# Optimization experiments

Hardware: AMD Instinct MI355X
Metric: run time of the kernel (lower is better)

Reference implementation:

```python
import jax, jax.numpy as jnp
import numpy as np


def setup_inputs() -> dict:
    key = jax.random.key(0)
    k0, k1, k2 = jax.random.split(key, 3)
    B, N, C = 2, 2048, 1024
    x = jax.random.normal(k0, (B, N, C), jnp.float32)
    W_qkv = jax.random.normal(k1, (3 * C, C), jnp.float32) * 0.02
    b_qkv = jnp.zeros((3 * C,), jnp.float32)
    W_out = jax.random.normal(k2, (C, C), jnp.float32) * 0.02
    b_out = jnp.zeros((C,), jnp.float32)
    return {"x": x, "W_qkv": W_qkv, "b_qkv": b_qkv, "W_out": W_out, "b_out": b_out, "n_heads": 16}


def reference(x, W_qkv, b_qkv, W_out, b_out, n_heads):
    B, N, C = x.shape
    dk = C // n_heads
    scale = 1.0 / np.sqrt(dk)
    # qkv projection -> (3, B, H, N, dk)
    qkv = (x @ W_qkv.T + b_qkv).reshape(B, N, 3, n_heads, dk).transpose(2, 0, 3, 1, 4)
    q, k, v = qkv[0], qkv[1], qkv[2]
    attn_all = jnp.einsum('bhqd,bhkd->bhqk', q, k) * scale  # (B,H,N,N)
    # sparsity measure per query row: max - mean
    M = jnp.max(attn_all, axis=-1) - jnp.mean(attn_all, axis=-1)  # (B,H,N)
    n_top = max(1, min(int(N * 0.25), N - 1))
    _, top_idx = jax.lax.top_k(M, n_top)  # (B,H,n_top)
    # keep[b,h,q] = True iff query row q is among top rows (vectorized scatter,
    # replaces the original per-(b,h) python loop)
    b_idx = jnp.arange(B)[:, None, None]
    h_idx = jnp.arange(n_heads)[None, :, None]
    keep = jnp.zeros((B, n_heads, N), bool).at[b_idx, h_idx, top_idx].set(True)
    # non-top query rows are fully masked to -1e9 (as in masked_fill)
    attn = jnp.where(keep[..., None], attn_all, jnp.float32(-1e9))
    attn = jax.nn.softmax(attn, axis=-1)
    # dropout is identity in eval mode
    out = jnp.einsum('bhqk,bhkd->bhqd', attn, v)
    out = out.transpose(0, 2, 1, 3).reshape(B, N, C)
    return out @ W_out.T + b_out
```

## Files before the change

kernel.cpp:

```cpp
#include <hip/hip_runtime.h>
#include <math.h>

typedef unsigned short u16;
typedef __attribute__((ext_vector_type(8))) short short8v;
typedef __attribute__((ext_vector_type(4))) float f32x4;

constexpr int B  = 2;
constexpr int N  = 2048;
constexpr int C  = 1024;
constexpr int H  = 16;
constexpr int DK = 64;
constexpr int NTOP = 512;
constexpr float SCALE = 0.125f;
constexpr int   BAND_CAP = 1024;
constexpr float BAND_EPS = 2e-3f;
constexpr int   CSEG = 16;

__device__ __forceinline__ void gload16(const u16* g, u16* l) {
    __builtin_amdgcn_global_load_lds(
        (const __attribute__((address_space(1))) unsigned int*)g,
        (__attribute__((address_space(3))) unsigned int*)l,
        16, 0, 0);
}

__device__ __forceinline__ u16 bf16_rne(float x) {
    unsigned u = __float_as_uint(x);
    unsigned r = u + 0x7fffu + ((u >> 16) & 1u);
    return (u16)(r >> 16);
}

__global__ __launch_bounds__(256) void convert_hilo(
    const float* __restrict__ src, u16* __restrict__ hi, u16* __restrict__ lo, int n)
{
    int i = (blockIdx.x * 256 + threadIdx.x) * 4;
    if (i >= n) return;
    float4 v = *(const float4*)&src[i];
    u16 h0 = bf16_rne(v.x), h1 = bf16_rne(v.y), h2 = bf16_rne(v.z), h3 = bf16_rne(v.w);
    float f0 = __uint_as_float((unsigned)h0 << 16);
    float f1 = __uint_as_float((unsigned)h1 << 16);
    float f2 = __uint_as_float((unsigned)h2 << 16);
    float f3 = __uint_as_float((unsigned)h3 << 16);
    *(ushort4*)&hi[i] = make_ushort4(h0, h1, h2, h3);
    *(ushort4*)&lo[i] = make_ushort4(bf16_rne(v.x - f0), bf16_rne(v.y - f1),
                                     bf16_rne(v.z - f2), bf16_rne(v.w - f3));
}

__global__ __launch_bounds__(256) void convert_hilo2(
    const float* __restrict__ a, const float* __restrict__ b,
    u16* __restrict__ ah, u16* __restrict__ al,
    u16* __restrict__ bh_, u16* __restrict__ bl_, int n)
{
    const float* src = blockIdx.y ? b : a;
    u16* hi = blockIdx.y ? bh_ : ah;
    u16* lo = blockIdx.y ? bl_ : al;
    int i = (blockIdx.x * 256 + threadIdx.x) * 4;
    if (i >= n) return;
    float4 v = *(const float4*)&src[i];
    u16 h0 = bf16_rne(v.x), h1 = bf16_rne(v.y), h2 = bf16_rne(v.z), h3 = bf16_rne(v.w);
    float f0 = __uint_as_float((unsigned)h0 << 16);
    float f1 = __uint_as_float((unsigned)h1 << 16);
    float f2 = __uint_as_float((unsigned)h2 << 16);
    float f3 = __uint_as_float((unsigned)h3 << 16);
    *(ushort4*)&hi[i] = make_ushort4(h0, h1, h2, h3);
    *(ushort4*)&lo[i] = make_ushort4(bf16_rne(v.x - f0), bf16_rne(v.y - f1),
                                     bf16_rne(v.z - f2), bf16_rne(v.w - f3));
}

__global__ __launch_bounds__(256) void convert_hilo_T(
    const float* __restrict__ v, u16* __restrict__ th, u16* __restrict__ tl)
{
    constexpr int LS = 68;
    __shared__ u16 Sh[64 * LS], Sl[64 * LS];
    const int bh = blockIdx.y;
    const int kt = blockIdx.x * 64;
    const int tid = threadIdx.x;
    #pragma unroll
    for (int p = 0; p < 4; ++p) {
        int idx = tid * 4 + p * 1024;
        int key = idx >> 6, d = idx & 63;
        float4 x4 = *(const float4*)&v[((size_t)bh * N + kt + key) * DK + d];
        float xs[4] = {x4.x, x4.y, x4.z, x4.w};
        ushort4 hh, ll;
        u16* hp = (u16*)&hh; u16* lp = (u16*)&ll;
        #pragma unroll
        for (int j = 0; j < 4; ++j) {
            u16 h = bf16_rne(xs[j]);
            hp[j] = h;
            lp[j] = bf16_rne(xs[j] - __uint_as_float((unsigned)h << 16));
        }
        *(ushort4*)&Sh[key * LS + d] = hh;
        *(ushort4*)&Sl[key * LS + d] = ll;
    }
    __syncthreads();
    const int d = tid >> 2, seg = tid & 3;
    u16 bufh[16], bufl[16];
    #pragma unroll
    for (int i = 0; i < 16; ++i) {
        bufh[i] = Sh[(seg * 16 + i) * LS + d];
        bufl[i] = Sl[(seg * 16 + i) * LS + d];
    }
    size_t oa = ((size_t)bh * DK + d) * N + kt + seg * 16;
    *(uint4*)&th[oa] = ((uint4*)bufh)[0];
    *(uint4*)&th[oa + 8] = ((uint4*)bufh)[1];
    *(uint4*)&tl[oa] = ((uint4*)bufl)[0];
    *(uint4*)&tl[oa + 8] = ((uint4*)bufl)[1];
}

template <int MODE>
__global__ __launch_bounds__(256) void gemm_mfma(
    const u16* __restrict__ Ahi, const u16* __restrict__ Alo,
    const u16* __restrict__ Bhi, const u16* __restrict__ Blo,
    const float* __restrict__ bias, float* __restrict__ out,
    float* __restrict__ qb, float* __restrict__ kb, float* __restrict__ vb,
    int K, int ntx)
{
    __shared__ __align__(16) u16 Ah[128 * 32], Al[128 * 32];
    __shared__ __align__(16) u16 Bh[128 * 32], Bl[128 * 32];

    const int nwg = gridDim.x;
    const int cpx = nwg >> 3;
    const int bid = blockIdx.x;
    const int swz = (bid & 7) * cpx + (bid >> 3);
    const int m0 = (swz / ntx) * 128;
    const int n0 = (swz % ntx) * 128;

    const int tid = threadIdx.x;
    const int lane = tid & 63;
    const int wave = tid >> 6;
    const int wr = wave >> 1, wc = wave & 1;
    const int fr = lane & 15, sl = lane >> 4;

    const u16* gsrc = (wave == 0) ? Ahi + (size_t)m0 * K
                    : (wave == 1) ? Alo + (size_t)m0 * K
                    : (wave == 2) ? Bhi + (size_t)n0 * K
                                  : Blo + (size_t)n0 * K;
    u16* lbase = (wave == 0) ? Ah : (wave == 1) ? Al : (wave == 2) ? Bh : Bl;

    f32x4 acc[4][4] = {};

    for (int k0 = 0; k0 < K; k0 += 32) {
        __syncthreads();
        #pragma unroll
        for (int i = 0; i < 8; ++i) {
            int c = i * 64 + lane;
            int row = c >> 2, sp = c & 3;
            int gs = sp ^ ((row >> 1) & 3);
            gload16(gsrc + (size_t)row * K + k0 + gs * 8, lbase + i * 512);
        }
        __syncthreads();

        short8v afh[4], afl[4], bfh[4], bfl[4];
        #pragma unroll
        for (int m = 0; m < 4; ++m) {
            int row = wr * 64 + m * 16 + fr;
            int off = row * 32 + ((sl ^ ((row >> 1) & 3)) * 8);
            afh[m] = *(const short8v*)&Ah[off];
            afl[m] = *(const short8v*)&Al[off];
        }
        #pragma unroll
        for (int n = 0; n < 4; ++n) {
            int row = wc * 64 + n * 16 + fr;
            int off = row * 32 + ((sl ^ ((row >> 1) & 3)) * 8);
            bfh[n] = *(const short8v*)&Bh[off];
            bfl[n] = *(const short8v*)&Bl[off];
        }
        #pragma unroll
        for (int m = 0; m < 4; ++m)
            #pragma unroll
            for (int n = 0; n < 4; ++n) {
                acc[m][n] = __builtin_amdgcn_mfma_f32_16x16x32_bf16(afh[m], bfh[n], acc[m][n], 0, 0, 0);
                acc[m][n] = __builtin_amdgcn_mfma_f32_16x16x32_bf16(afh[m], bfl[n], acc[m][n], 0, 0, 0);
                acc[m][n] = __builtin_amdgcn_mfma_f32_16x16x32_bf16(afl[m], bfh[n], acc[m][n], 0, 0, 0);
            }
    }

    #pragma unroll
    for (int m = 0; m < 4; ++m)
        #pragma unroll
        for (int n = 0; n < 4; ++n)
            #pragma unroll
            for (int r = 0; r < 4; ++r) {
                int grow = m0 + wr * 64 + m * 16 + sl * 4 + r;
                int gcol = n0 + wc * 64 + n * 16 + fr;
                float val = acc[m][n][r] + bias[gcol];
                if (MODE == 0) {
                    int t = gcol >> 10, h = (gcol >> 6) & 15, d = gcol & 63;
                    int bb = grow >> 11, nn = grow & (N - 1);
                    float* dst = (t == 0) ? qb : (t == 1) ? kb : vb;
                    dst[(((size_t)bb * H + h) * N + nn) * DK + d] = val;
                } else {
                    out[(size_t)grow * C + gcol] = val;
                }
            }
}

__global__ __launch_bounds__(256) void colsum_part2(
    const float* __restrict__ v, const float* __restrict__ k,
    float* __restrict__ partial)
{
    const int bh = blockIdx.y, seg = blockIdx.x, which = blockIdx.z;
    const float* src = which ? k : v;
    const int d = threadIdx.x & 63;
    const int sub = threadIdx.x >> 6;
    const int k0 = seg * (N / CSEG);
    float s = 0.f;
    for (int kk = sub; kk < N / CSEG; kk += 4)
        s += src[((size_t)bh * N + k0 + kk) * DK + d];
    __shared__ float part[4][64];
    part[sub][d] = s;
    __syncthreads();
    if (threadIdx.x < 64)
        partial[(((size_t)which * B * H + bh) * CSEG + seg) * DK + d] =
            part[0][d] + part[1][d] + part[2][d] + part[3][d];
}

__global__ __launch_bounds__(128) void colsum_final2(
    const float* __restrict__ partial, float* __restrict__ vmean,
    float* __restrict__ kmean)
{
    const int bh = blockIdx.x;
    const int d = threadIdx.x & 63;
    const int which = threadIdx.x >> 6;
    const float* p = partial + ((size_t)which * B * H + bh) * CSEG * DK;
    float s = 0.f;
    #pragma unroll
    for (int g = 0; g < CSEG; ++g) s += p[g * DK + d];
    float* dst = which ? kmean : vmean;
    dst[bh * DK + d] = s / (float)N;
}

__global__ __launch_bounds__(256) void qdot_kernel(
    const float* __restrict__ q, const float* __restrict__ kmean,
    float* __restrict__ Mdot)
{
    const int bh = blockIdx.y;
    const int row = blockIdx.x * 256 + threadIdx.x;
    __shared__ float km[DK];
    if (threadIdx.x < DK) km[threadIdx.x] = kmean[bh * DK + threadIdx.x];
    __syncthreads();
    const float* qr = &q[((size_t)bh * N + row) * DK];
    float s = 0.f;
    #pragma unroll
    for (int d4 = 0; d4 < DK; d4 += 4) {
        float4 v = *(const float4*)&qr[d4];
        s += v.x * km[d4] + v.y * km[d4 + 1] + v.z * km[d4 + 2] + v.w * km[d4 + 3];
    }
    Mdot[(size_t)bh * N + row] = s;
}

__global__ __launch_bounds__(256) void row_stats_mfma(
    const u16* __restrict__ qh_, const u16* __restrict__ ql_,
    const u16* __restrict__ kh_, const u16* __restrict__ kl_,
    const float* __restrict__ Mdot, float* __restrict__ Mout,
    float* __restrict__ rowmax)
{
    __shared__ __align__(16) u16 Kh[64 * 64];
    __shared__ __align__(16) u16 Kl[64 * 64];
    const int tid = threadIdx.x, lane = tid & 63, wave = tid >> 6;

    const int nwg = gridDim.x;
    const int cpx = nwg >> 3;
    const int bid = blockIdx.x;
    const int swz = (bid & 7) * cpx + (bid >> 3);
    const int bh = swz >> 4;
    const int q0 = (swz & 15) * 128 + wave * 32;
    const int fr = lane & 15, g = lane >> 4;

    const u16* gsrc = (wave & 2) ? kl_ : kh_;
    u16* lbase = (wave & 2) ? Kl : Kh;
    const int cb = (wave & 1) * 256;

    short8v qfh[2][2], qfl[2][2];
    #pragma unroll
    for (int m = 0; m < 2; ++m)
        #pragma unroll
        for (int kk = 0; kk < 2; ++kk) {
            size_t qa = ((size_t)bh * N + q0 + m * 16 + fr) * DK + kk * 32 + g * 8;
            qfh[m][kk] = *(const short8v*)&qh_[qa];
            qfl[m][kk] = *(const short8v*)&ql_[qa];
        }

    f32x4 mx[2];
    mx[0] = (f32x4){-1e30f, -1e30f, -1e30f, -1e30f};
    mx[1] = mx[0];

    for (int kt = 0; kt < N; kt += 64) {
        __syncthreads();
        #pragma unroll
        for (int i = 0; i < 4; ++i) {
            int c = cb + i * 64 + lane;
            int row = c >> 3, sp = c & 7;
            int gs = sp ^ (row & 7);
            gload16(gsrc + ((size_t)bh * N + kt + row) * DK + gs * 8,
                    lbase + (size_t)(cb + i * 64) * 8);
        }
        __syncthreads();
        short8v bfh[4][2], bfl[4][2];
        #pragma unroll
        for (int n = 0; n < 4; ++n)
            #pragma unroll
            for (int kk = 0; kk < 2; ++kk) {
                int key = n * 16 + fr;
                int off = key * 64 + (((g + kk * 4) ^ (key & 7)) * 8);
                bfh[n][kk] = *(const short8v*)&Kh[off];
                bfl[n][kk] = *(const short8v*)&Kl[off];
            }
        #pragma unroll
        for (int m = 0; m < 2; ++m)
            #pragma unroll
            for (int n = 0; n < 4; ++n) {
                f32x4 a = {};
                #pragma unroll
                for (int kk = 0; kk < 2; ++kk) {
                    a = __builtin_amdgcn_mfma_f32_16x16x32_bf16(qfl[m][kk], bfh[n][kk], a, 0, 0, 0);
                    a = __builtin_amdgcn_mfma_f32_16x16x32_bf16(qfh[m][kk], bfl[n][kk], a, 0, 0, 0);
                    a = __builtin_amdgcn_mfma_f32_16x16x32_bf16(qfh[m][kk], bfh[n][kk], a, 0, 0, 0);
                }
                #pragma unroll
                for (int r = 0; r < 4; ++r) mx[m][r] = fmaxf(mx[m][r], a[r]);
            }
    }

    #pragma unroll
    for (int w = 1; w < 16; w <<= 1)
        #pragma unroll
        for (int m = 0; m < 2; ++m)
            #pragma unroll
            for (int r = 0; r < 4; ++r)
                mx[m][r] = fmaxf(mx[m][r], __shfl_xor(mx[m][r], w, 64));

    if (fr == 0) {
        #pragma unroll
        for (int m = 0; m < 2; ++m)
            #pragma unroll
            for (int r = 0; r < 4; ++r) {
                int row = q0 + m * 16 + g * 4 + r;
                size_t idx = (size_t)bh * N + row;
                float v = mx[m][r];
                rowmax[idx] = SCALE * v;
                Mout[idx]   = SCALE * (v - Mdot[idx]);
            }
    }
}

__global__ __launch_bounds__(256) void topk_thr(
    const float* __restrict__ Mv, float* __restrict__ thr, int* __restrict__ cnt)
{
    const int bh = blockIdx.y;
    const int qi = blockIdx.x * 256 + threadIdx.x;
    if (blockIdx.x == 0 && threadIdx.x == 0) cnt[bh] = 0;
    __shared__ float Ms[N];
    for (int e = threadIdx.x; e < N; e += 256) Ms[e] = Mv[(size_t)bh * N + e];
    __syncthreads();
    const float mq = Ms[qi];
    int rank = 0;
    for (int j = 0; j < N; ++j) {
        float mj = Ms[j];
        rank += (mj > mq) || (mj == mq && j < qi);
    }
    if (rank == NTOP - 1) thr[bh] = mq;
}

__global__ __launch_bounds__(256) void band_classify(
    const float* __restrict__ Mv, const float* __restrict__ thr,
    int* __restrict__ cnt, int* __restrict__ band, int* __restrict__ keep)
{
    const int bh = blockIdx.y;
    const int row = blockIdx.x * 256 + threadIdx.x;
    const float m = Mv[(size_t)bh * N + row];
    const float t = thr[bh];
    int kp;
    if (fabsf(m - t) <= BAND_EPS) {
        int pos = atomicAdd(&cnt[bh], 1);
        if (pos < BAND_CAP) band[bh * BAND_CAP + pos] = row;
        kp = 0;
    } else {
        kp = (m > t) ? 1 : 0;
    }
    keep[(size_t)bh * N + row] = kp;
}

__global__ __launch_bounds__(256) void refine_kernel(
    const float* __restrict__ q, const float* __restrict__ k,
    const int* __restrict__ cnt, const int* __restrict__ band,
    float* __restrict__ Mv)
{
    constexpr int LS = 69;
    __shared__ float Ks[64 * LS];
    __shared__ float qs[DK];
    const int bh = blockIdx.y;
    const int tid = threadIdx.x;
    const int n = min(cnt[bh], BAND_CAP);
    for (int ci = blockIdx.x; ci < n; ci += 32) {
        const int row = band[bh * BAND_CAP + ci];
        __syncthreads();
        if (tid < DK) qs[tid] = q[((size_t)bh * N + row) * DK + tid];
        double mx = -1e30, sm = 0.0;
        for (int kt = 0; kt < N; kt += 64) {
            __syncthreads();
            #pragma unroll
            for (int p = 0; p < 4; ++p) {
                int idx = tid * 4 + p * 1024;
                int kr = idx >> 6, d = idx & 63;
                float4 x4 = *(const float4*)&k[((size_t)bh * N + kt + kr) * DK + d];
                Ks[kr * LS + d]     = x4.x;
                Ks[kr * LS + d + 1] = x4.y;
                Ks[kr * LS + d + 2] = x4.z;
                Ks[kr * LS + d + 3] = x4.w;
            }
            __syncthreads();
            if (tid < 64) {
                double s = 0.0;
                #pragma unroll
                for (int d = 0; d < DK; ++d)
                    s += (double)qs[d] * (double)Ks[tid * LS + d];
                mx = fmax(mx, s);
                sm += s;
            }
        }
        if (tid < 64) {
            #pragma unroll
            for (int w = 1; w < 64; w <<= 1) {
                mx = fmax(mx, __shfl_xor(mx, w, 64));
                sm += __shfl_xor(sm, w, 64);
            }
            if (tid == 0)
                Mv[(size_t)bh * N + row] = (float)((double)SCALE * (mx - sm / (double)N));
        }
    }
}

__global__ __launch_bounds__(256) void band_finalize(
    const float* __restrict__ Mv, const int* __restrict__ cnt,
    const int* __restrict__ band, int* __restrict__ keep,
    int* __restrict__ kidx)
{
    __shared__ unsigned char kL[N];
    __shared__ int   bRow[BAND_CAP];
    __shared__ float bM[BAND_CAP];
    __shared__ int aW[4];
    __shared__ int scan[256];

    const int bh = blockIdx.x;
    const int tid = threadIdx.x;
    const int lane = tid & 63, wid = tid >> 6;
    const int nb = min(cnt[bh], BAND_CAP);

    int above = 0;
    #pragma unroll
    for (int w = 0; w < 8; ++w) {
        int row = w * 256 + tid;
        int kp = keep[(size_t)bh * N + row];
        kL[row] = (unsigned char)kp;
        above += kp;
    }
    #pragma unroll
    for (int w = 1; w < 64; w <<= 1) above += __shfl_xor(above, w, 64);
    if (lane == 0) aW[wid] = above;
    for (int i = tid; i < nb; i += 256) {
        int r = band[bh * BAND_CAP + i];
        bRow[i] = r;
        bM[i] = Mv[(size_t)bh * N + r];
    }
    __syncthreads();
    const int nAbove = aW[0] + aW[1] + aW[2] + aW[3];

    for (int i = tid; i < nb; i += 256) {
        const float mi = bM[i];
        const int ri = bRow[i];
        int rank = nAbove;
        for (int j = 0; j < nb; ++j) {
            float mj = bM[j];
            rank += (mj > mi) || (mj == mi && bRow[j] < ri);
        }
        int kp = (rank < NTOP) ? 1 : 0;
        kL[ri] = (unsigned char)kp;
        keep[(size_t)bh * N + ri] = kp;
    }
    __syncthreads();

    int cntL = 0;
    #pragma unroll
    for (int r = 0; r < 8; ++r) cntL += kL[tid * 8 + r];
    scan[tid] = cntL;
    __syncthreads();
    for (int s = 1; s < 256; s <<= 1) {
        int v = (tid >= s) ? scan[tid - s] : 0;
        __syncthreads();
        scan[tid] += v;
        __syncthreads();
    }
    int pos = scan[tid] - cntL;
    #pragma unroll
    for (int r = 0; r < 8; ++r) {
        int row = tid * 8 + r;
        if (kL[row]) kidx[bh * NTOP + pos++] = row;
    }
}

__global__ __launch_bounds__(256) void fill_nonkept(
    const int* __restrict__ keep, const float* __restrict__ vmean,
    float* __restrict__ attn_out)
{
    const int bh = blockIdx.y;
    const int b = bh >> 4, h = bh & 15;
    const int d = threadIdx.x & 63;
    const int rr = threadIdx.x >> 6;
    const float vm = vmean[bh * DK + d];
    #pragma unroll
    for (int i = 0; i < 16; ++i) {
        int row = blockIdx.x * 64 + i * 4 + rr;
        if (!keep[(size_t)bh * N + row])
            attn_out[((size_t)b * N + row) * C + h * DK + d] = vm;
    }
}

__global__ __launch_bounds__(256) void attn_mfma(
    const u16* __restrict__ qh_, const u16* __restrict__ ql_,
    const u16* __restrict__ kh_, const u16* __restrict__ kl_,
    const u16* __restrict__ vth_, const u16* __restrict__ vtl_,
    const float* __restrict__ rowmax, const int* __restrict__ kidx,
    float* __restrict__ attn_out)
{
    __shared__ __align__(16) u16 Kh[64 * 64], Kl[64 * 64];
    __shared__ __align__(16) u16 Vh[64 * 64], Vl[64 * 64];
    __shared__ __align__(16) u16 Ph[4][16 * 64], Pl[4][16 * 64];

    const int tid = threadIdx.x, lane = tid & 63, wave = tid >> 6;
    const int wg = blockIdx.x;
    const int bh = ((wg >> 6) << 3) | (wg & 7);
    const int xblk = (wg >> 3) & 7;
    const int b = bh >> 4, h = bh & 15;
    const int q0 = xblk * 64 + wave * 16;
    const int fr = lane & 15, sl = lane >> 4;

    const bool isV = (wave >= 2);
    const u16* ksrc = (wave & 1) ? kl_ : kh_;
    const u16* vsrc = (wave & 1) ? vtl_ : vth_;
    u16* lbase = (wave == 0) ? Kh : (wave == 1) ? Kl : (wave == 2) ? Vh : Vl;
    const size_t kbase0 = (size_t)bh * N * DK;
    const size_t vbase0 = (size_t)bh * DK * N;

    const int* kix = kidx + bh * NTOP;
    const int qrow_f = kix[q0 + fr];
    int qr_o[4]; float rmax_r[4];
    #pragma unroll
    for (int r = 0; r < 4; ++r) {
        qr_o[r] = kix[q0 + sl * 4 + r];
        rmax_r[r] = rowmax[(size_t)bh * N + qr_o[r]];
    }

    short8v qfh[2], qfl[2];
    #pragma unroll
    for (int kk = 0; kk < 2; ++kk) {
        size_t qa = ((size_t)bh * N + qrow_f) * DK + kk * 32 + sl * 8;
        qfh[kk] = *(const short8v*)&qh_[qa];
        qfl[kk] = *(const short8v*)&ql_[qa];
    }

    f32x4 opv[4] = {};
    float lsum[4] = {};

    for (int kt = 0; kt < N; kt += 64) {
        __syncthreads();
        #pragma unroll
        for (int i = 0; i < 8; ++i) {
            int c = i * 64 + lane;
            int row = c >> 3, sp = c & 7;
            int gs = sp ^ (row & 7);
            const u16* g = isV ? (vsrc + vbase0 + (size_t)row * N + kt + gs * 8)
                               : (ksrc + kbase0 + (size_t)(kt + row) * DK + gs * 8);
            gload16(g, lbase + (size_t)i * 512);
        }
        __syncthreads();

        #pragma unroll
        for (int n = 0; n < 4; ++n) {
            f32x4 a = {};
            __builtin_amdgcn_s_setprio(1);
            #pragma unroll
            for (int kk = 0; kk < 2; ++kk) {
                int key = n * 16 + fr;
                int off = key * 64 + (((sl + kk * 4) ^ (key & 7)) * 8);
                short8v bh_f = *(const short8v*)&Kh[off];
                short8v bl_f = *(const short8v*)&Kl[off];
                a = __builtin_amdgcn_mfma_f32_16x16x32_bf16(qfl[kk], bh_f, a, 0, 0, 0);
                a = __builtin_amdgcn_mfma_f32_16x16x32_bf16(qfh[kk], bl_f, a, 0, 0, 0);
                a = __builtin_amdgcn_mfma_f32_16x16x32_bf16(qfh[kk], bh_f, a, 0, 0, 0);
            }
            __builtin_amdgcn_s_setprio(0);
            #pragma unroll
            for (int r = 0; r < 4; ++r) {
                float p = __expf(a[r] * SCALE - rmax_r[r]);
                lsum[r] += p;
                u16 ph = bf16_rne(p);
                u16 pl = bf16_rne(p - __uint_as_float((unsigned)ph << 16));
                int q_l = sl * 4 + r;
                int key = n * 16 + fr;
                int off = q_l * 64 + (((key >> 3) ^ (q_l & 7)) * 8) + (key & 7);
                Ph[wave][off] = ph;
                Pl[wave][off] = pl;
            }
        }

        __builtin_amdgcn_s_setprio(1);
        #pragma unroll
        for (int kk = 0; kk < 2; ++kk) {
            int aoff = fr * 64 + (((kk * 4 + sl) ^ (fr & 7)) * 8);
            short8v pah = *(const short8v*)&Ph[wave][aoff];
            short8v pal = *(const short8v*)&Pl[wave][aoff];
            #pragma unroll
            for (int n = 0; n < 4; ++n) {
                int d = n * 16 + fr;
                int voff = d * 64 + (((kk * 4 + sl) ^ (d & 7)) * 8);
                short8v vhf = *(const short8v*)&Vh[voff];
                short8v vlf = *(const short8v*)&Vl[voff];
                opv[n] = __builtin_amdgcn_mfma_f32_16x16x32_bf16(pal, vhf, opv[n], 0, 0, 0);
                opv[n] = __builtin_amdgcn_mfma_f32_16x16x32_bf16(pah, vlf, opv[n], 0, 0, 0);
                opv[n] = __builtin_amdgcn_mfma_f32_16x16x32_bf16(pah, vhf, opv[n], 0, 0, 0);
            }
        }
        __builtin_amdgcn_s_setprio(0);
    }

    #pragma unroll
    for (int w = 1; w < 16; w <<= 1)
        #pragma unroll
        for (int r = 0; r < 4; ++r)
            lsum[r] += __shfl_xor(lsum[r], w, 64);

    #pragma unroll
    for (int r = 0; r < 4; ++r) {
        const float inv = 1.0f / lsum[r];
        float* orow = attn_out + ((size_t)b * N + qr_o[r]) * C + h * DK;
        #pragma unroll
        for (int n = 0; n < 4; ++n)
            orow[n * 16 + fr] = opv[n][r] * inv;
    }
}

extern "C" void kernel_launch(void* const* d_in, const int* in_sizes, int n_in,
                              void* d_out, int out_size, void* d_ws, size_t ws_size,
                              hipStream_t stream)
{
    const float* x    = (const float*)d_in[0];
    const float* Wqkv = (const float*)d_in[1];
    const float* bqkv = (const float*)d_in[2];
    const float* Wout = (const float*)d_in[3];
    const float* bout = (const float*)d_in[4];
    float* out = (float*)d_out;

    char* ws = (char*)d_ws;
    size_t off = 0;
    auto alloc = [&](size_t bytes) -> void* {
        void* p = ws + off;
        off += (bytes + 255) & ~(size_t)255;
        return p;
    };

    const size_t BHND = (size_t)B * H * N * DK;
    float* q        = (float*)alloc(BHND * 4);
    float* kbuf     = (float*)alloc(BHND * 4);
    float* vbuf     = (float*)alloc(BHND * 4);
    float* attn_out = (float*)alloc((size_t)B * N * C * 4);
    u16* cvAhi = (u16*)alloc((size_t)B * N * C * 2);
    u16* cvAlo = (u16*)alloc((size_t)B * N * C * 2);
    u16* cvBhi = (u16*)alloc((size_t)3 * C * C * 2);
    u16* cvBlo = (u16*)alloc((size_t)3 * C * C * 2);
    u16* qhi   = (u16*)alloc(BHND * 2);
    u16* qlo   = (u16*)alloc(BHND * 2);
    u16* khi   = (u16*)alloc(BHND * 2);
    u16* klo   = (u16*)alloc(BHND * 2);
    u16* vthi  = (u16*)alloc(BHND * 2);
    u16* vtlo  = (u16*)alloc(BHND * 2);
    float* Mbuf     = (float*)alloc((size_t)B * H * N * 4);
    float* rmaxbuf  = (float*)alloc((size_t)B * H * N * 4);
    float* Mdot     = (float*)alloc((size_t)B * H * N * 4);
    int*   keep     = (int*)  alloc((size_t)B * H * N * 4);
    int*   kidx     = (int*)  alloc((size_t)B * H * NTOP * 4);
    float* vmeanbuf = (float*)alloc((size_t)B * H * DK * 4);
    float* kmeanbuf = (float*)alloc((size_t)B * H * DK * 4);
    float* partbuf  = (float*)alloc((size_t)2 * B * H * CSEG * DK * 4);
    float* thrbuf   = (float*)alloc((size_t)B * H * 4);
    int*   cntbuf   = (int*)  alloc((size_t)B * H * 4);
    int*   bandbuf  = (int*)  alloc((size_t)B * H * BAND_CAP * 4);

    const int nX = B * N * C;
    const int nW = 3 * C * C;
    const int nWo = C * C;

    convert_hilo<<<nX / 1024, 256, 0, stream>>>(x, cvAhi, cvAlo, nX);
    convert_hilo<<<nW / 1024, 256, 0, stream>>>(Wqkv, cvBhi, cvBlo, nW);

    gemm_mfma<0><<<768, 256, 0, stream>>>(
        cvAhi, cvAlo, cvBhi, cvBlo, bqkv, nullptr, q, kbuf, vbuf, C, 24);

    convert_hilo2<<<dim3(nX / 1024, 2), 256, 0, stream>>>(
        q, kbuf, qhi, qlo, khi, klo, nX);
    convert_hilo_T<<<dim3(N / 64, B * H), 256, 0, stream>>>(vbuf, vthi, vtlo);

    colsum_part2<<<dim3(CSEG, B * H, 2), 256, 0, stream>>>(vbuf, kbuf, partbuf);
    colsum_final2<<<B * H, 128, 0, stream>>>(partbuf, vmeanbuf, kmeanbuf);

    qdot_kernel<<<dim3(N / 256, B * H), 256, 0, stream>>>(q, kmeanbuf, Mdot);

    row_stats_mfma<<<512, 256, 0, stream>>>(
        qhi, qlo, khi, klo, Mdot, Mbuf, rmaxbuf);

    topk_thr<<<dim3(N / 256, B * H), 256, 0, stream>>>(Mbuf, thrbuf, cntbuf);
    band_classify<<<dim3(N / 256, B * H), 256, 0, stream>>>(Mbuf, thrbuf, cntbuf, bandbuf, keep);
    refine_kernel<<<dim3(32, B * H), 256, 0, stream>>>(q, kbuf, cntbuf, bandbuf, Mbuf);
    band_finalize<<<B * H, 256, 0, stream>>>(Mbuf, cntbuf, bandbuf, keep, kidx);

    fill_nonkept<<<dim3(N / 64, B * H), 256, 0, stream>>>(keep, vmeanbuf, attn_out);
    attn_mfma<<<256, 256, 0, stream>>>(
        qhi, qlo, khi, klo, vthi, vtlo, rmaxbuf, kidx, attn_out);

    convert_hilo<<<nX / 1024, 256, 0, stream>>>(attn_out, cvAhi, cvAlo, nX);
    convert_hilo<<<nWo / 1024, 256, 0, stream>>>(Wout, cvBhi, cvBlo, nWo);
    gemm_mfma<1><<<256, 256, 0, stream>>>(
        cvAhi, cvAlo, cvBhi, cvBlo, bout, out, nullptr, nullptr, nullptr, C, 8);
}
```

Measured before the change: 405.7 us.

## Batch band refinement per head and drop XCD block swizzling

The refine kernel now uses one block per batch-head instead of 32 strided blocks. Each block processes 32 candidate rows together, with 8 threads per candidate, so each loaded K tile is reused across many query rows. Before, one row was handled per pass with only 64 active threads. Separately, the GEMM and row_stats kernels drop the XCD-aware blockIdx swizzle in favour of plain 2D grids, which may hurt L2 locality across the chiplets. The refine change reduces redundant K loads but runs only 32 blocks, so it uses less of the GPU.

```diff
diff --git a/kernel.cpp b/kernel.cpp
--- a/kernel.cpp
+++ b/kernel.cpp
@@ -112,19 +112,14 @@
     const u16* __restrict__ Bhi, const u16* __restrict__ Blo,
     const float* __restrict__ bias, float* __restrict__ out,
     float* __restrict__ qb, float* __restrict__ kb, float* __restrict__ vb,
-    int K, int ntx)
+    int K)
 {
     __shared__ __align__(16) u16 Ah[128 * 32], Al[128 * 32];
     __shared__ __align__(16) u16 Bh[128 * 32], Bl[128 * 32];
 
-    const int nwg = gridDim.x;
-    const int cpx = nwg >> 3;
-    const int bid = blockIdx.x;
-    const int swz = (bid & 7) * cpx + (bid >> 3);
-    const int m0 = (swz / ntx) * 128;
-    const int n0 = (swz % ntx) * 128;
-
     const int tid = threadIdx.x;
+    const int m0 = blockIdx.y * 128;
+    const int n0 = blockIdx.x * 128;
     const int lane = tid & 63;
     const int wave = tid >> 6;
     const int wr = wave >> 1, wc = wave & 1;
@@ -257,13 +252,8 @@
     __shared__ __align__(16) u16 Kh[64 * 64];
     __shared__ __align__(16) u16 Kl[64 * 64];
     const int tid = threadIdx.x, lane = tid & 63, wave = tid >> 6;
-
-    const int nwg = gridDim.x;
-    const int cpx = nwg >> 3;
-    const int bid = blockIdx.x;
-    const int swz = (bid & 7) * cpx + (bid >> 3);
-    const int bh = swz >> 4;
-    const int q0 = (swz & 15) * 128 + wave * 32;
+    const int bh = blockIdx.y;
+    const int q0 = blockIdx.x * 128 + wave * 32;
     const int fr = lane & 15, g = lane >> 4;
 
     const u16* gsrc = (wave & 2) ? kl_ : kh_;
@@ -380,21 +370,27 @@
     keep[(size_t)bh * N + row] = kp;
 }
 
-__global__ __launch_bounds__(256) void refine_kernel(
+__global__ __launch_bounds__(256) void refine_kernel2(
     const float* __restrict__ q, const float* __restrict__ k,
     const int* __restrict__ cnt, const int* __restrict__ band,
     float* __restrict__ Mv)
 {
     constexpr int LS = 69;
     __shared__ float Ks[64 * LS];
-    __shared__ float qs[DK];
-    const int bh = blockIdx.y;
+    __shared__ float qs[32][DK];
+    const int bh = blockIdx.x;
     const int tid = threadIdx.x;
-    const int n = min(cnt[bh], BAND_CAP);
-    for (int ci = blockIdx.x; ci < n; ci += 32) {
-        const int row = band[bh * BAND_CAP + ci];
-        __syncthreads();
-        if (tid < DK) qs[tid] = q[((size_t)bh * N + row) * DK + tid];
+    const int nb = min(cnt[bh], BAND_CAP);
+    const int cand = tid >> 3;
+    const int kg = tid & 7;
+
+    for (int c0 = 0; c0 < nb; c0 += 32) {
+        const int nc = min(32, nb - c0);
+        __syncthreads();
+        for (int e = tid; e < nc * DK; e += 256) {
+            int ci = e >> 6, d = e & 63;
+            qs[ci][d] = q[((size_t)bh * N + band[bh * BAND_CAP + c0 + ci]) * DK + d];
+        }
         double mx = -1e30, sm = 0.0;
         for (int kt = 0; kt < N; kt += 64) {
             __syncthreads();
@@ -409,23 +405,28 @@
                 Ks[kr * LS + d + 3] = x4.w;
             }
             __syncthreads();
-            if (tid < 64) {
-                double s = 0.0;
+            if (cand < nc) {
                 #pragma unroll
-                for (int d = 0; d < DK; ++d)
-                    s += (double)qs[d] * (double)Ks[tid * LS + d];
-                mx = fmax(mx, s);
-                sm += s;
-            }
-        }
-        if (tid < 64) {
-            #pragma unroll
-            for (int w = 1; w < 64; w <<= 1) {
-                mx = fmax(mx, __shfl_xor(mx, w, 64));
-                sm += __shfl_xor(sm, w, 64);
-            }
-            if (tid == 0)
-                Mv[(size_t)bh * N + row] = (float)((double)SCALE * (mx - sm / (double)N));
+                for (int j = 0; j < 8; ++j) {
+                    const int key = kg * 8 + j;
+                    double s = 0.0;
+                    #pragma unroll
+                    for (int d = 0; d < DK; ++d)
+                        s += (double)qs[cand][d] * (double)Ks[key * LS + d];
+                    mx = fmax(mx, s);
+                    sm += s;
+                }
+            }
+        }
+        #pragma unroll
+        for (int w = 1; w < 8; w <<= 1) {
+            mx = fmax(mx, __shfl_xor(mx, w, 64));
+            sm += __shfl_xor(sm, w, 64);
+        }
+        if (kg == 0 && cand < nc) {
+            const int row = band[bh * BAND_CAP + c0 + cand];
+            Mv[(size_t)bh * N + row] =
+                (float)((double)SCALE * (mx - sm / (double)N));
         }
     }
 }
@@ -692,8 +693,8 @@
     convert_hilo<<<nX / 1024, 256, 0, stream>>>(x, cvAhi, cvAlo, nX);
     convert_hilo<<<nW / 1024, 256, 0, stream>>>(Wqkv, cvBhi, cvBlo, nW);
 
-    gemm_mfma<0><<<768, 256, 0, stream>>>(
-        cvAhi, cvAlo, cvBhi, cvBlo, bqkv, nullptr, q, kbuf, vbuf, C, 24);
+    gemm_mfma<0><<<dim3(3 * C / 128, (B * N) / 128), 256, 0, stream>>>(
+        cvAhi, cvAlo, cvBhi, cvBlo, bqkv, nullptr, q, kbuf, vbuf, C);
 
     convert_hilo2<<<dim3(nX / 1024, 2), 256, 0, stream>>>(
         q, kbuf, qhi, qlo, khi, klo, nX);
@@ -704,12 +705,12 @@
 
     qdot_kernel<<<dim3(N / 256, B * H), 256, 0, stream>>>(q, kmeanbuf, Mdot);
 
-    row_stats_mfma<<<512, 256, 0, stream>>>(
+    row_stats_mfma<<<dim3(N / 128, B * H), 256, 0, stream>>>(
         qhi, qlo, khi, klo, Mdot, Mbuf, rmaxbuf);
 
     topk_thr<<<dim3(N / 256, B * H), 256, 0, stream>>>(Mbuf, thrbuf, cntbuf);
     band_classify<<<dim3(N / 256, B * H), 256, 0, stream>>>(Mbuf, thrbuf, cntbuf, bandbuf, keep);
-    refine_kernel<<<dim3(32, B * H), 256, 0, stream>>>(q, kbuf, cntbuf, bandbuf, Mbuf);
+    refine_kernel2<<<B * H, 256, 0, stream>>>(q, kbuf, cntbuf, bandbuf, Mbuf);
     band_finalize<<<B * H, 256, 0, stream>>>(Mbuf, cntbuf, bandbuf, keep, kidx);
 
     fill_nonkept<<<dim3(N / 64, B * H), 256, 0, stream>>>(keep, vmeanbuf, attn_out);
@@ -718,6 +719,6 @@
 
     convert_hilo<<<nX / 1024, 256, 0, stream>>>(attn_out, cvAhi, cvAlo, nX);
     convert_hilo<<<nWo / 1024, 256, 0, stream>>>(Wout, cvBhi, cvBlo, nWo);
-    gemm_mfma<1><<<256, 256, 0, stream>>>(
-        cvAhi, cvAlo, cvBhi, cvBlo, bout, out, nullptr, nullptr, nullptr, C, 8);
-}
+    gemm_mfma<1><<<dim3(C / 128, (B * N) / 128), 256, 0, stream>>>(
+        cvAhi, cvAlo, cvBhi, cvBlo, bout, out, nullptr, nullptr, nullptr, C);
+}
```

New measurement: 485.6 us. 1.2x slower.
